# Kernel optimization log

Hardware: AMD Instinct MI355X
Metric: run time of the kernel (lower is better)

Reference implementation:

```python
import jax, jax.numpy as jnp
import numpy as np

# ---- configuration (matches init_kwargs) ----
B, C_IO, T = 2, 64, 4096
PATCH = 2
W0, W1 = 512, 1024           # widths
D_DN, D_MID = 2, 4           # depths per level
DH = 64                      # dim per head
WIN = 128                    # local attention window
MAP = 1024                   # mapping_dim
DFF_MAP = 1024               # mapping_d_ff
FF_MULT = 2                  # GEGLU ff_mult in local levels
H_DN = W0 // DH              # 8 heads
H_MID = W1 // DH             # 16 heads


def _n(key, shape, s=0.02):
    return jax.random.normal(key, shape, jnp.float32) * s


def setup_inputs() -> dict:
    key = jax.random.key(0)
    ks = iter(jax.random.split(key, 64))
    p = {}
    p['x'] = jax.random.normal(next(ks), (B, C_IO, T), jnp.float32)
    p['t'] = jax.random.uniform(next(ks), (B,), jnp.float32)
    p['time_w'] = jax.random.normal(next(ks), (MAP // 2, 1), jnp.float32)
    p['time_in_w'] = _n(next(ks), (MAP, MAP))
    p['map_in_s'] = jnp.ones((MAP,), jnp.float32)
    p['map_norm_s'] = jnp.ones((2, MAP), jnp.float32)
    p['map_up_w'] = _n(next(ks), (2, MAP, 2 * DFF_MAP))
    p['map_down_w'] = _n(next(ks), (2, DFF_MAP, MAP))
    p['map_out_s'] = jnp.ones((MAP,), jnp.float32)
    p['patch_in_w'] = _n(next(ks), (C_IO * PATCH, W0))
    p['dn_anorm_w'] = _n(next(ks), (D_DN, MAP, W0))
    p['dn_qkv_w'] = _n(next(ks), (D_DN, W0, 3 * W0))
    p['dn_o_w'] = _n(next(ks), (D_DN, W0, W0))
    p['dn_fnorm_w'] = _n(next(ks), (D_DN, MAP, W0))
    p['dn_ff1_w'] = _n(next(ks), (D_DN, W0, 2 * FF_MULT * W0))
    p['dn_ff2_w'] = _n(next(ks), (D_DN, FF_MULT * W0, W0))
    p['merge_w'] = _n(next(ks), (W0 * 2, W1))
    p['mid_map_w'] = _n(next(ks), (MAP, W1))
    p['mid_pin_w'] = _n(next(ks), (W1, W1))
    p['mid_pout_w'] = _n(next(ks), (W1, W1))
    p['mid_ln1_g'] = jnp.ones((D_MID, W1), jnp.float32)
    p['mid_ln1_b'] = jnp.zeros((D_MID, W1), jnp.float32)
    p['mid_qkv_w'] = _n(next(ks), (D_MID, W1, 3 * W1))
    p['mid_o_w'] = _n(next(ks), (D_MID, W1, W1))
    p['mid_ln2_g'] = jnp.ones((D_MID, W1), jnp.float32)
    p['mid_ln2_b'] = jnp.zeros((D_MID, W1), jnp.float32)
    p['mid_ff1_w'] = _n(next(ks), (D_MID, W1, 8 * W1))
    p['mid_ff2_w'] = _n(next(ks), (D_MID, 4 * W1, W1))
    p['mid_fn_g'] = jnp.ones((W1,), jnp.float32)
    p['mid_fn_b'] = jnp.zeros((W1,), jnp.float32)
    p['split_w'] = _n(next(ks), (W1, W0 * 2))
    p['split_fac'] = jnp.full((1,), 0.5, jnp.float32)
    p['up_anorm_w'] = _n(next(ks), (D_DN, MAP, W0))
    p['up_qkv_w'] = _n(next(ks), (D_DN, W0, 3 * W0))
    p['up_o_w'] = _n(next(ks), (D_DN, W0, W0))
    p['up_fnorm_w'] = _n(next(ks), (D_DN, MAP, W0))
    p['up_ff1_w'] = _n(next(ks), (D_DN, W0, 2 * FF_MULT * W0))
    p['up_ff2_w'] = _n(next(ks), (D_DN, FF_MULT * W0, W0))
    p['out_norm_s'] = jnp.ones((W0,), jnp.float32)
    p['patch_out_w'] = _n(next(ks), (W0, C_IO * PATCH))
    return p


def rmsnorm(x, scale, eps=1e-6):
    ms = jnp.mean(jnp.square(x), -1, keepdims=True)
    return x * (scale * jax.lax.rsqrt(ms + eps))


def layernorm(x, g, b, eps=1e-5):
    m = jnp.mean(x, -1, keepdims=True)
    v = jnp.mean(jnp.square(x - m), -1, keepdims=True)
    return (x - m) * jax.lax.rsqrt(v + eps) * g + b


def rope_tables(S, D):
    inv = 1.0 / (10000.0 ** (jnp.arange(0, D, 2, dtype=jnp.float32) / D))
    ang = jnp.arange(S, dtype=jnp.float32)[:, None] * inv  # [S, D/2]
    return jnp.cos(ang), jnp.sin(ang)


def apply_rope(x, cos, sin):
    # x: [B,H,S,D], contiguous-half rotation
    x1, x2 = jnp.split(x, 2, -1)
    return jnp.concatenate([x1 * cos - x2 * sin, x2 * cos + x1 * sin], -1)


def heads_split(x, h):
    Bx, S, C = x.shape
    return x.reshape(Bx, S, h, C // h).transpose(0, 2, 1, 3)


def heads_merge(x):
    Bx, h, S, D = x.shape
    return x.transpose(0, 2, 1, 3).reshape(Bx, S, h * D)


def local_attn(q, k, v, w):
    # non-causal sliding-window attention: each query window attends to
    # [prev, self, next] windows (look_backward=1, look_forward=1)
    Bx, H, S, D = q.shape
    nw = S // w
    qw = q.reshape(Bx, H, nw, w, D)
    def ctx(tn):
        tw = tn.reshape(Bx, H, nw, w, D)
        pad = jnp.pad(tw, ((0, 0), (0, 0), (1, 1), (0, 0), (0, 0)))
        return jnp.concatenate([pad[:, :, :-2], pad[:, :, 1:-1], pad[:, :, 2:]], 3)  # [B,H,nw,3w,D]
    kw, vw = ctx(k), ctx(v)
    s = jnp.einsum('bhnqd,bhnkd->bhnqk', qw * (D ** -0.5), kw)
    valid = jnp.ones((nw, 3 * w), bool).at[0, :w].set(False).at[-1, 2 * w:].set(False)
    s = jnp.where(valid[None, None, :, None, :], s, jnp.finfo(s.dtype).min)
    a = jax.nn.softmax(s, -1)
    return jnp.einsum('bhnqk,bhnkd->bhnqd', a, vw).reshape(Bx, H, S, D)


def token_merge(x, w, r=2):
    # 'b (n r) c -> b n (c r)' then linear
    Bx, S, C = x.shape
    x = x.reshape(Bx, S // r, r, C).transpose(0, 1, 3, 2).reshape(Bx, S // r, C * r)
    return x @ w


def token_split(x, w, r=2):
    # linear then 'b n (c r) -> b (n r) c'
    y = x @ w
    Bx, n, CR = y.shape
    C = CR // r
    return y.reshape(Bx, n, C, r).transpose(0, 1, 3, 2).reshape(Bx, n * r, C)


def mapping(e, in_s, norm_s, up_w, down_w, out_s):
    x = rmsnorm(e, in_s)
    for l in range(up_w.shape[0]):
        h = rmsnorm(x, norm_s[l])
        a, g = jnp.split(h @ up_w[l], 2, -1)
        x = x + (a * jax.nn.gelu(g)) @ down_w[l]
    return rmsnorm(x, out_s)


def local_level(x, cond, anorm, qkv_w, o_w, fnorm, ff1, ff2, heads, win):
    Bx, S, C = x.shape
    D = C // heads
    cos, sin = rope_tables(S, D)
    for l in range(qkv_w.shape[0]):
        h = rmsnorm(x, 1.0 + (cond @ anorm[l])[:, None, :])  # AdaRMSNorm
        q, k, v = jnp.split(h @ qkv_w[l], 3, -1)
        q, k, v = heads_split(q, heads), heads_split(k, heads), heads_split(v, heads)
        q, k = apply_rope(q, cos, sin), apply_rope(k, cos, sin)
        x = x + heads_merge(local_attn(q, k, v, win)) @ o_w[l]
        h = rmsnorm(x, 1.0 + (cond @ fnorm[l])[:, None, :])
        a, g = jnp.split(h @ ff1[l], 2, -1)
        x = x + (a * jax.nn.gelu(g)) @ ff2[l]  # GEGLU FF
    return x


def mid_level(x, ln1g, ln1b, qkv_w, o_w, ln2g, ln2b, ff1, ff2, fng, fnb, heads):
    Bx, S, C = x.shape
    D = C // heads
    cos, sin = rope_tables(S, D)
    for l in range(qkv_w.shape[0]):
        h = layernorm(x, ln1g[l], ln1b[l])
        q, k, v = jnp.split(h @ qkv_w[l], 3, -1)
        q, k, v = heads_split(q, heads), heads_split(k, heads), heads_split(v, heads)
        q, k = apply_rope(q, cos, sin), apply_rope(k, cos, sin)
        s = jnp.einsum('bhqd,bhkd->bhqk', q * (D ** -0.5), k)
        o = jnp.einsum('bhqk,bhkd->bhqd', jax.nn.softmax(s, -1), v)
        x = x + heads_merge(o) @ o_w[l]
        h = layernorm(x, ln2g[l], ln2b[l])
        a, g = jnp.split(h @ ff1[l], 2, -1)
        x = x + (a * jax.nn.silu(g)) @ ff2[l]  # SwiGLU FF
    return layernorm(x, fng, fnb)


def _forward(x, t, time_w, time_in_w, map_in_s, map_norm_s, map_up_w, map_down_w, map_out_s,
             patch_in_w, dn_anorm_w, dn_qkv_w, dn_o_w, dn_fnorm_w, dn_ff1_w, dn_ff2_w,
             merge_w, mid_map_w, mid_pin_w, mid_pout_w, mid_ln1_g, mid_ln1_b, mid_qkv_w,
             mid_o_w, mid_ln2_g, mid_ln2_b, mid_ff1_w, mid_ff2_w, mid_fn_g, mid_fn_b,
             split_w, split_fac, up_anorm_w, up_qkv_w, up_o_w, up_fnorm_w, up_ff1_w,
             up_ff2_w, out_norm_s, patch_out_w):
    h = jnp.swapaxes(x, 1, 2)                      # [B,T,C_io]
    h = token_merge(h, patch_in_w, PATCH)          # [B, T/2, W0]
    f = 2.0 * jnp.pi * (t[:, None] @ time_w.T)     # Fourier features
    temb = jnp.concatenate([jnp.cos(f), jnp.sin(f)], -1) @ time_in_w
    cond = mapping(temb, map_in_s, map_norm_s, map_up_w, map_down_w, map_out_s)  # [B,MAP]
    h = local_level(h, cond, dn_anorm_w, dn_qkv_w, dn_o_w, dn_fnorm_w, dn_ff1_w, dn_ff2_w, H_DN, WIN)
    skip = h
    h = token_merge(h, merge_w)                    # [B, T/4, W1]
    h = h @ mid_pin_w
    pre = (cond @ mid_map_w)[:, None, :]           # prepended mapping token
    h = jnp.concatenate([pre, h], 1)
    h = mid_level(h, mid_ln1_g, mid_ln1_b, mid_qkv_w, mid_o_w, mid_ln2_g, mid_ln2_b,
                  mid_ff1_w, mid_ff2_w, mid_fn_g, mid_fn_b, H_MID)
    h = (h @ mid_pout_w)[:, 1:, :]
    h = token_split(h, split_w)                    # back to [B, T/2, W0]
    h = skip + split_fac * (h - skip)              # lerp skip fusion
    h = local_level(h, cond, up_anorm_w, up_qkv_w, up_o_w, up_fnorm_w, up_ff1_w, up_ff2_w, H_DN, WIN)
    h = rmsnorm(h, out_norm_s)
    h = token_split(h, patch_out_w, PATCH)         # [B,T,C_io]
    return jnp.swapaxes(h, 1, 2)


def reference(x, t, time_w, time_in_w, map_in_s, map_norm_s, map_up_w, map_down_w, map_out_s,
              patch_in_w, dn_anorm_w, dn_qkv_w, dn_o_w, dn_fnorm_w, dn_ff1_w, dn_ff2_w,
              merge_w, mid_map_w, mid_pin_w, mid_pout_w, mid_ln1_g, mid_ln1_b, mid_qkv_w,
              mid_o_w, mid_ln2_g, mid_ln2_b, mid_ff1_w, mid_ff2_w, mid_fn_g, mid_fn_b,
              split_w, split_fac, up_anorm_w, up_qkv_w, up_o_w, up_fnorm_w, up_ff1_w,
              up_ff2_w, out_norm_s, patch_out_w):
    return _forward(x, t, time_w, time_in_w, map_in_s, map_norm_s, map_up_w, map_down_w, map_out_s,
                    patch_in_w, dn_anorm_w, dn_qkv_w, dn_o_w, dn_fnorm_w, dn_ff1_w, dn_ff2_w,
                    merge_w, mid_map_w, mid_pin_w, mid_pout_w, mid_ln1_g, mid_ln1_b, mid_qkv_w,
                    mid_o_w, mid_ln2_g, mid_ln2_b, mid_ff1_w, mid_ff2_w, mid_fn_g, mid_fn_b,
                    split_w, split_fac, up_anorm_w, up_qkv_w, up_o_w, up_fnorm_w, up_ff1_w,
                    up_ff2_w, out_norm_s, patch_out_w)
```

## Files before the change

kernel.cpp:

```cpp
#include <hip/hip_runtime.h>
#include <math.h>

#define BB   2
#define CIO  64
#define TT   4096
#define S0   2048
#define W0   512
#define HDN  8
#define SM   1025
#define SMP  1088
#define W1   1024
#define HMID 16
#define WIN  128
#define NW   16
#define MAPD 1024
#define KSPL 16
#define PKCAP 8396800L

typedef _Float16 f16;
typedef _Float16 half8 __attribute__((ext_vector_type(8)));
typedef _Float16 half4v __attribute__((ext_vector_type(4)));
typedef _Float16 half2v __attribute__((ext_vector_type(2)));
typedef float floatx4 __attribute__((ext_vector_type(4)));

__device__ __forceinline__ float gelu_tanh(float x) {
    float x3 = x * x * x;
    return 0.5f * x * (1.f + tanhf(0.7978845608028654f * (x + 0.044715f * x3)));
}

__global__ __launch_bounds__(256) void wcast(
    const float* __restrict__ W, f16* __restrict__ Wt, int K, int N) {
    __shared__ float T[64][65];
    const int n0 = blockIdx.x * 64, k0 = blockIdx.y * 64;
    const int tid = threadIdx.x;
    for (int e = tid; e < 4096; e += 256) {
        int r = e >> 6, c = e & 63;
        T[r][c] = W[(size_t)(k0 + r) * N + n0 + c];
    }
    __syncthreads();
    for (int e = tid; e < 2048; e += 256) {
        int r = e >> 5, c2 = (e & 31) * 2;
        half2v p;
        p[0] = (f16)T[c2][r];
        p[1] = (f16)T[c2 + 1][r];
        *(half2v*)(Wt + (size_t)(n0 + r) * K + k0 + c2) = p;
    }
}

template<int OUTM>
__global__ __launch_bounds__(256) void gemm_h(
    const f16* __restrict__ A, const f16* __restrict__ Bt,
    const float* __restrict__ res, void* __restrict__ Cv,
    int M, int N, int K) {
    __shared__ __align__(16) f16 As[3][4096];
    __shared__ __align__(16) f16 Bs[3][4096];
    const int tid = threadIdx.x;
    const int wv = tid >> 6, ln = tid & 63;
    int nwg = gridDim.x * gridDim.y;
    int orig = blockIdx.y * gridDim.x + blockIdx.x;
    int wg = orig;
    if (nwg >= 16) {
        int q = nwg >> 3, r = nwg & 7;
        int xcd = orig & 7, lot = orig >> 3;
        wg = (xcd < r ? xcd * (q + 1) : r * (q + 1) + (xcd - r) * q) + lot;
    }
    const int bm = (wg / gridDim.x) * 128, bn = (wg % gridDim.x) * 128;
    int Kc = K, kbase = 0;
    if (OUTM == 2) { Kc = K / gridDim.z; kbase = blockIdx.z * Kc; }
    const int nt = Kc >> 5;

    auto stage = [&](int buf, int kt) {
        int k0 = kbase + (kt << 5);
#pragma unroll
        for (int i = 0; i < 2; ++i) {
            int off = i * 4096 + wv * 1024 + ln * 16;
            int row = off >> 6, kb = (off & 63) >> 1;
            int gr = bm + row; gr = gr < M ? gr : M - 1;
            f16* gp = const_cast<f16*>(A) + (size_t)gr * K + k0 + kb;
            __builtin_amdgcn_global_load_lds(
                (__attribute__((address_space(1))) void*)gp,
                (__attribute__((address_space(3))) void*)(&As[buf][i * 2048 + wv * 512]),
                16, 0, 0);
            f16* gq = const_cast<f16*>(Bt) + (size_t)(bn + row) * K + k0 + kb;
            __builtin_amdgcn_global_load_lds(
                (__attribute__((address_space(1))) void*)gq,
                (__attribute__((address_space(3))) void*)(&Bs[buf][i * 2048 + wv * 512]),
                16, 0, 0);
        }
    };

    floatx4 acc[4][4];
#pragma unroll
    for (int m = 0; m < 4; ++m)
#pragma unroll
        for (int n = 0; n < 4; ++n) acc[m][n] = (floatx4)0.f;
    const int r = ln & 15, kc = (ln >> 4) * 8;
    const int wr = (wv >> 1) * 64, wc = (wv & 1) * 64;

    stage(0, 0);
    if (nt > 1) stage(1, 1);
    int buf = 0;
    for (int t = 0; t < nt; ++t) {
        if (t + 1 < nt) { asm volatile("s_waitcnt vmcnt(4)" ::: "memory"); }
        else            { asm volatile("s_waitcnt vmcnt(0)" ::: "memory"); }
        __builtin_amdgcn_s_barrier();
        if (t + 2 < nt) {
            int nb = buf + 2; if (nb >= 3) nb -= 3;
            stage(nb, t + 2);
        }
        half8 af[4], bf[4];
#pragma unroll
        for (int m = 0; m < 4; ++m)
            af[m] = *(const half8*)(&As[buf][(wr + m * 16 + r) * 32 + kc]);
#pragma unroll
        for (int n = 0; n < 4; ++n)
            bf[n] = *(const half8*)(&Bs[buf][(wc + n * 16 + r) * 32 + kc]);
#pragma unroll
        for (int m = 0; m < 4; ++m)
#pragma unroll
            for (int n = 0; n < 4; ++n)
                acc[m][n] = __builtin_amdgcn_mfma_f32_16x16x32_f16(af[m], bf[n], acc[m][n], 0, 0, 0);
        if (++buf >= 3) buf = 0;
    }

    float* Cf = (float*)Cv;
    f16*   Ch = (f16*)Cv;
    if (OUTM == 2) Cf += (size_t)blockIdx.z * M * N;
#pragma unroll
    for (int m = 0; m < 4; ++m) {
        int rbase = bm + wr + m * 16 + ((ln >> 4) << 2);
#pragma unroll
        for (int j = 0; j < 4; ++j) {
            int row = rbase + j;
            if (row < M) {
                size_t ro = (size_t)row * N;
#pragma unroll
                for (int n = 0; n < 4; ++n) {
                    int col = bn + wc + n * 16 + (ln & 15);
                    float v = acc[m][n][j];
                    if (OUTM == 1) Ch[ro + col] = (f16)v;
                    else if (OUTM == 0) Cf[ro + col] = v + (res ? res[ro + col] : 0.f);
                    else Cf[ro + col] = v;
                }
            }
        }
    }
}

__global__ __launch_bounds__(256) void gemm_qkv(
    const f16* __restrict__ A, const f16* __restrict__ Bt,
    const float* __restrict__ tab, f16* __restrict__ Fq,
    f16* __restrict__ Fk, f16* __restrict__ Fv,
    int M, int N, int K, int S, int H) {
    __shared__ __align__(16) f16 As[3][4096];
    __shared__ __align__(16) f16 Bs[3][4096];
    const int tid = threadIdx.x;
    const int wv = tid >> 6, ln = tid & 63;
    int nwg = gridDim.x * gridDim.y;
    int orig = blockIdx.y * gridDim.x + blockIdx.x;
    int wg = orig;
    if (nwg >= 16) {
        int q = nwg >> 3, r = nwg & 7;
        int xcd = orig & 7, lot = orig >> 3;
        wg = (xcd < r ? xcd * (q + 1) : r * (q + 1) + (xcd - r) * q) + lot;
    }
    const int bm = (wg / gridDim.x) * 128, bn = (wg % gridDim.x) * 128;
    const int nt = K >> 5;

    auto stage = [&](int buf, int kt) {
        int k0 = kt << 5;
#pragma unroll
        for (int i = 0; i < 2; ++i) {
            int off = i * 4096 + wv * 1024 + ln * 16;
            int row = off >> 6, kb = (off & 63) >> 1;
            int gr = bm + row; gr = gr < M ? gr : M - 1;
            f16* gp = const_cast<f16*>(A) + (size_t)gr * K + k0 + kb;
            __builtin_amdgcn_global_load_lds(
                (__attribute__((address_space(1))) void*)gp,
                (__attribute__((address_space(3))) void*)(&As[buf][i * 2048 + wv * 512]),
                16, 0, 0);
            f16* gq = const_cast<f16*>(Bt) + (size_t)(bn + row) * K + k0 + kb;
            __builtin_amdgcn_global_load_lds(
                (__attribute__((address_space(1))) void*)gq,
                (__attribute__((address_space(3))) void*)(&Bs[buf][i * 2048 + wv * 512]),
                16, 0, 0);
        }
    };

    floatx4 acc[4][4];
#pragma unroll
    for (int m = 0; m < 4; ++m)
#pragma unroll
        for (int n = 0; n < 4; ++n) acc[m][n] = (floatx4)0.f;
    const int r = ln & 15, kc = (ln >> 4) * 8;
    const int wr = (wv >> 1) * 64, wc = (wv & 1) * 64;

    stage(0, 0);
    if (nt > 1) stage(1, 1);
    int buf = 0;
    for (int t = 0; t < nt; ++t) {
        if (t + 1 < nt) { asm volatile("s_waitcnt vmcnt(4)" ::: "memory"); }
        else            { asm volatile("s_waitcnt vmcnt(0)" ::: "memory"); }
        __builtin_amdgcn_s_barrier();
        if (t + 2 < nt) {
            int nb = buf + 2; if (nb >= 3) nb -= 3;
            stage(nb, t + 2);
        }
        half8 af[4], bf[4];
#pragma unroll
        for (int m = 0; m < 4; ++m)
            af[m] = *(const half8*)(&As[buf][(wr + m * 16 + r) * 32 + kc]);
#pragma unroll
        for (int n = 0; n < 4; ++n)
            bf[n] = *(const half8*)(&Bs[buf][(wc + n * 16 + r) * 32 + kc]);
#pragma unroll
        for (int m = 0; m < 4; ++m)
#pragma unroll
            for (int n = 0; n < 4; ++n)
                acc[m][n] = __builtin_amdgcn_mfma_f32_16x16x32_f16(af[m], bf[n], acc[m][n], 0, 0, 0);
        if (++buf >= 3) buf = 0;
    }

    const int C = N / 3;
    const int colbase = bn + wc;
    const int reg = colbase / C;
// ... 120 lines not shown
    }
    P[((size_t)blockIdx.y * 2 + 0) * tot + c] = acc0;
    P[((size_t)blockIdx.y * 2 + 1) * tot + c] = acc1;
}

__global__ __launch_bounds__(256) void gemv2L_red(
    const float* __restrict__ P, float* __restrict__ C, int Nper, int L) {
    int tot = L * Nper;
    int g = blockIdx.x * 256 + threadIdx.x;
    if (g >= 2 * tot) return;
    int m = g / tot, cc = g - m * tot;
    float s = 0.f;
#pragma unroll
    for (int ky = 0; ky < KSPL; ++ky)
        s += P[((size_t)ky * 2 + m) * tot + cc];
    int l = cc / Nper, n = cc - l * Nper;
    C[((size_t)l * 2 + m) * Nper + n] = s;
}

__device__ __forceinline__ void stf(float* p, float v) { *p = v; }
__device__ __forceinline__ void stf(f16* p, float v)   { *p = (f16)v; }

template<typename TO>
__global__ __launch_bounds__(256) void rmsnorm_k(
    const float* __restrict__ X, const float* __restrict__ scale,
    TO* __restrict__ Y, int C, int rows_per_group, float sadd) {
    int row = blockIdx.x, tid = threadIdx.x;
    const float* x = X + (size_t)row * C;
    float v[8];
    int cnt = C >> 8;
    float ss = 0.f;
    for (int i = 0; i < cnt; ++i) { v[i] = x[tid + (i << 8)]; ss += v[i] * v[i]; }
    __shared__ float red[256];
    red[tid] = ss; __syncthreads();
    for (int s2 = 128; s2; s2 >>= 1) { if (tid < s2) red[tid] += red[tid + s2]; __syncthreads(); }
    float inv = rsqrtf(red[0] / (float)C + 1e-6f);
    const float* sc = scale + (size_t)(row / rows_per_group) * C;
    TO* y = Y + (size_t)row * C;
    for (int i = 0; i < cnt; ++i) {
        int c = tid + (i << 8);
        stf(&y[c], v[i] * (sadd + sc[c]) * inv);
    }
}

__global__ __launch_bounds__(256) void layernorm_k(
    const float* __restrict__ X, const float* __restrict__ g,
    const float* __restrict__ bta, f16* __restrict__ Y, int C) {
    int row = blockIdx.x, tid = threadIdx.x;
    const float* x = X + (size_t)row * C;
    float v[8];
    int cnt = C >> 8;
    float s = 0.f;
    for (int i = 0; i < cnt; ++i) { v[i] = x[tid + (i << 8)]; s += v[i]; }
    __shared__ float red[256];
    red[tid] = s; __syncthreads();
    for (int s2 = 128; s2; s2 >>= 1) { if (tid < s2) red[tid] += red[tid + s2]; __syncthreads(); }
    float m = red[0] / (float)C;
    __syncthreads();
    float s2s = 0.f;
    for (int i = 0; i < cnt; ++i) { float d = v[i] - m; s2s += d * d; }
    red[tid] = s2s; __syncthreads();
    for (int s2 = 128; s2; s2 >>= 1) { if (tid < s2) red[tid] += red[tid + s2]; __syncthreads(); }
    float inv = rsqrtf(red[0] / (float)C + 1e-5f);
    f16* y = Y + (size_t)row * C;
    for (int i = 0; i < cnt; ++i) {
        int c = tid + (i << 8);
        y[c] = (f16)((v[i] - m) * inv * g[c] + bta[c]);
    }
}

__global__ __launch_bounds__(256) void glu_k(
    const float* __restrict__ U, float* __restrict__ Yo,
    size_t total, int F, int mode) {
    size_t gidx = (size_t)blockIdx.x * 256 + threadIdx.x;
    if (gidx >= total) return;
    size_t r = gidx / (size_t)F;
    int c = (int)(gidx - r * F);
    const float* u = U + r * (size_t)(2 * F);
    float a = u[c], gg = u[F + c];
    float act = (mode == 0) ? gelu_tanh(gg) : gg / (1.f + expf(-gg));
    Yo[gidx] = a * act;
}

__global__ __launch_bounds__(256) void glu_h8(
    const f16* __restrict__ U, f16* __restrict__ Yo,
    size_t total8, int F8, int mode) {
    size_t gi = (size_t)blockIdx.x * 256 + threadIdx.x;
    if (gi >= total8) return;
    size_t r = gi / (size_t)F8;
    int c = (int)(gi - r * (size_t)F8);
    const f16* u = U + r * (size_t)F8 * 16;
    half8 av = *(const half8*)(u + c * 8);
    half8 gv = *(const half8*)(u + F8 * 8 + c * 8);
    half8 y;
#pragma unroll
    for (int j = 0; j < 8; ++j) {
        float a = (float)av[j], gg = (float)gv[j];
        float act = (mode == 0) ? gelu_tanh(gg) : gg / (1.f + __expf(-gg));
        y[j] = (f16)(a * act);
    }
    *(half8*)(Yo + gi * 8) = y;
}

__global__ __launch_bounds__(256) void vtrans(
    const f16* __restrict__ V, f16* __restrict__ Vt, int S, int Spad) {
    __shared__ f16 T[64][72];
    const int tid = threadIdx.x;
    const int k0 = blockIdx.x * 64;
    const f16* Vb = V + (size_t)blockIdx.y * S * 64;
    f16* Vtb = Vt + (size_t)blockIdx.y * 64 * Spad;
    for (int c = tid; c < 512; c += 256) {
        int kk = c >> 3, d8 = (c & 7) * 8;
        int kg = k0 + kk; kg = kg < S ? kg : S - 1;
        half8 v = *(const half8*)(Vb + (size_t)kg * 64 + d8);
        if (k0 + kk >= S) {
#pragma unroll
            for (int j = 0; j < 8; ++j) v[j] = (f16)0.f;
        }
        *(half8*)(&T[kk][d8]) = v;
    }
    __syncthreads();
    for (int c = tid; c < 512; c += 256) {
        int d = c >> 3, k8 = (c & 7) * 8;
        half8 o;
#pragma unroll
        for (int j = 0; j < 8; ++j) o[j] = T[k8 + j][d];
        *(half8*)(Vtb + (size_t)d * Spad + k0 + k8) = o;
    }
}

__global__ __launch_bounds__(256) void fattn(
    const f16* __restrict__ Q, const f16* __restrict__ K,
    const f16* __restrict__ Vt, float* __restrict__ Op,
    float* __restrict__ Mst, float* __restrict__ Lst,
    int S, int Spad, int H, int win, int QR) {
    __shared__ __align__(16) f16 Ks[64][72];
    __shared__ __align__(16) f16 Vs[64][72];
    __shared__ __align__(16) f16 Ps[4][32][72];
    const int tid = threadIdx.x;
    const int wv = tid >> 6, ln = tid & 63;
    const int r15 = ln & 15, g = ln >> 4;
    const int bh = blockIdx.y;
    const int NBH = gridDim.y;
    const int z = blockIdx.z, nz = gridDim.z;
    const int q0 = (int)blockIdx.x * 128;
    const f16* Qb = Q + (size_t)bh * S * 64;
    const f16* Kb = K + (size_t)bh * S * 64;
    const f16* Vtb = Vt + (size_t)bh * 64 * Spad;

    half8 aq[2][2];
#pragma unroll
    for (int m = 0; m < 2; ++m) {
        int q = q0 + wv * 32 + m * 16 + r15;
        q = q < S ? q : S - 1;
#pragma unroll
        for (int ks = 0; ks < 2; ++ks)
            aq[m][ks] = *(const half8*)(Qb + (size_t)q * 64 + ks * 32 + g * 8);
    }
    floatx4 o[2][4];
#pragma unroll
    for (int m = 0; m < 2; ++m)
#pragma unroll
        for (int n = 0; n < 4; ++n) o[m][n] = (floatx4)0.f;
    float mst[2][4], lst[2][4];
#pragma unroll
    for (int m = 0; m < 2; ++m)
#pragma unroll
        for (int j = 0; j < 4; ++j) { mst[m][j] = -3.0e38f; lst[m][j] = 0.f; }

    int klo = 0, khi = S;
    if (win) {
        int n = (int)blockIdx.x;
        klo = (n - 1) * win; if (klo < 0) klo = 0;
        khi = (n + 2) * win; if (khi > S) khi = S;
    }
    int ntile = (khi - klo + 63) >> 6;
    int chunk = (ntile + nz - 1) / nz;
    int myLo = klo + z * chunk * 64;
    int myHi = klo + (z + 1) * chunk * 64; if (myHi > khi) myHi = khi;

    for (int kb = myLo; kb < myHi; kb += 64) {
        __syncthreads();
#pragma unroll
        for (int i = 0; i < 2; ++i) {
            int c = tid + i * 256;
            int rr = c >> 3, c8 = (c & 7) * 8;
            int kg = kb + rr; kg = kg < S ? kg : S - 1;
            *(half8*)(&Ks[rr][c8]) = *(const half8*)(Kb + (size_t)kg * 64 + c8);
            *(half8*)(&Vs[rr][c8]) = *(const half8*)(Vtb + (size_t)rr * Spad + kb + c8);
        }
        __syncthreads();
        floatx4 s[2][4];
#pragma unroll
        for (int m = 0; m < 2; ++m)
#pragma unroll
            for (int n = 0; n < 4; ++n) s[m][n] = (floatx4)0.f;
#pragma unroll
        for (int ks = 0; ks < 2; ++ks) {
            half8 bk[4];
#pragma unroll
            for (int n = 0; n < 4; ++n)
                bk[n] = *(const half8*)(&Ks[n * 16 + r15][ks * 32 + g * 8]);
#pragma unroll
            for (int m = 0; m < 2; ++m)
#pragma unroll
                for (int n = 0; n < 4; ++n)
                    s[m][n] = __builtin_amdgcn_mfma_f32_16x16x32_f16(aq[m][ks], bk[n], s[m][n], 0, 0, 0);
        }
        if (kb + 64 > S) {
#pragma unroll
            for (int n = 0; n < 4; ++n)
                if (kb + n * 16 + r15 >= S) {
#pragma unroll
                    for (int m = 0; m < 2; ++m) s[m][n] = (floatx4)(-3.0e38f);
                }
        }
#pragma unroll
        for (int m = 0; m < 2; ++m) {
#pragma unroll
            for (int j = 0; j < 4; ++j) {
                float tm = fmaxf(fmaxf(s[m][0][j], s[m][1][j]), fmaxf(s[m][2][j], s[m][3][j]));
                tm = fmaxf(tm, __shfl_xor(tm, 1));
                tm = fmaxf(tm, __shfl_xor(tm, 2));
                tm = fmaxf(tm, __shfl_xor(tm, 4));
                tm = fmaxf(tm, __shfl_xor(tm, 8));
                float mn = fmaxf(mst[m][j], tm);
                float sc = __expf(mst[m][j] - mn);
                mst[m][j] = mn;
                float ts = 0.f;
#pragma unroll
                for (int n = 0; n < 4; ++n) {
                    float p = __expf(s[m][n][j] - mn);
                    s[m][n][j] = p;
                    ts += p;
                }
                ts += __shfl_xor(ts, 1);
                ts += __shfl_xor(ts, 2);
                ts += __shfl_xor(ts, 4);
                ts += __shfl_xor(ts, 8);
                lst[m][j] = lst[m][j] * sc + ts;
#pragma unroll
                for (int n = 0; n < 4; ++n) o[m][n][j] *= sc;
            }
        }
#pragma unroll
        for (int m = 0; m < 2; ++m)
#pragma unroll
            for (int n = 0; n < 4; ++n)
#pragma unroll
                for (int j = 0; j < 4; ++j)
                    Ps[wv][m * 16 + g * 4 + j][n * 16 + r15] = (f16)s[m][n][j];
#pragma unroll
        for (int ks = 0; ks < 2; ++ks) {
            half8 pa[2], bv[4];
#pragma unroll
            for (int m = 0; m < 2; ++m)
                pa[m] = *(const half8*)(&Ps[wv][m * 16 + r15][ks * 32 + g * 8]);
#pragma unroll
            for (int n = 0; n < 4; ++n)
                bv[n] = *(const half8*)(&Vs[n * 16 + r15][ks * 32 + g * 8]);
#pragma unroll
            for (int m = 0; m < 2; ++m)
#pragma unroll
                for (int n = 0; n < 4; ++n)
                    o[m][n] = __builtin_amdgcn_mfma_f32_16x16x32_f16(pa[m], bv[n], o[m][n], 0, 0, 0);
        }
    }
    size_t zb = ((size_t)z * NBH + bh) * QR;
#pragma unroll
    for (int m = 0; m < 2; ++m)
#pragma unroll
        for (int j = 0; j < 4; ++j) {
            int qr = q0 + wv * 32 + m * 16 + g * 4 + j;
            size_t ro = (zb + qr) * 64;
#pragma unroll
            for (int n = 0; n < 4; ++n)
                Op[ro + n * 16 + r15] = o[m][n][j];
            if (r15 == 0) {
                Mst[zb + qr] = mst[m][j];
                Lst[zb + qr] = lst[m][j];
            }
        }
}

__global__ __launch_bounds__(256) void fcomb(
    const float* __restrict__ Op, const float* __restrict__ Mst,
    const float* __restrict__ Lst, f16* __restrict__ O,
    int S, int H, int QR, int nz, int rows) {
    int g = blockIdx.x * 256 + threadIdx.x;
    int idx = g >> 4;
    int d4 = (g & 15) * 4;
    if (idx >= rows) return;
    int bh = idx / QR, q = idx - bh * QR;
    if (q >= S) return;
    float mstar = -3.0e38f;
    for (int z = 0; z < nz; ++z)
        mstar = fmaxf(mstar, Mst[(size_t)z * rows + idx]);
    float den = 0.f;
    floatx4 num = (floatx4)0.f;
    for (int z = 0; z < nz; ++z) {
        float w = __expf(Mst[(size_t)z * rows + idx] - mstar);
        den += w * Lst[(size_t)z * rows + idx];
        floatx4 ov = *(const floatx4*)(Op + ((size_t)z * rows + idx) * 64 + d4);
        num += w * ov;
    }
    float inv = 1.f / den;
    int b = bh / H, h = bh % H;
    f16* op = O + ((size_t)b * S + q) * (H * 64) + h * 64 + d4;
    half4v hv;
#pragma unroll
    for (int j = 0; j < 4; ++j) hv[j] = (f16)(num[j] * inv);
    *(half4v*)op = hv;
}

__global__ __launch_bounds__(256) void patch_in_gather(
    const float* __restrict__ x, f16* __restrict__ out) {
    int g = blockIdx.x * 256 + threadIdx.x;
    if (g >= BB * S0 * 128) return;
    int k = g & 127;
    int n = (g >> 7) & (S0 - 1);
    int b = g >> 18;
    out[g] = (f16)x[(size_t)b * CIO * TT + (size_t)(k >> 1) * TT + 2 * n + (k & 1)];
}

__global__ __launch_bounds__(256) void time_embed(
    const float* __restrict__ t, const float* __restrict__ tw,
    float* __restrict__ te) {
    int g = blockIdx.x * 256 + threadIdx.x;
    if (g >= BB * MAPD) return;
    int b = g / MAPD, j = g % MAPD;
    float w = tw[(j < 512) ? j : j - 512];
    float ang = 6.283185307179586f * t[b] * w;
    te[g] = (j < 512) ? cosf(ang) : sinf(ang);
}

__global__ __launch_bounds__(256) void token_merge_gather(
    const float* __restrict__ A, f16* __restrict__ out) {
    int g = blockIdx.x * 256 + threadIdx.x;
    if (g >= BB * 1024 * 1024) return;
    int k = g & 1023;
    int n = (g >> 10) & 1023;
    int b = g >> 20;
    out[g] = (f16)A[((size_t)b * S0 + 2 * n + (k & 1)) * W0 + (k >> 1)];
}

__global__ __launch_bounds__(256) void concat_mid(
    const float* __restrict__ pre, const float* __restrict__ Dsrc,
    float* __restrict__ Cm) {
    int g = blockIdx.x * 256 + threadIdx.x;
    if (g >= BB * SM * W1) return;
    int c = g & 1023;
    int row = g >> 10;
    int b = row / SM, r = row % SM;
    Cm[g] = (r == 0) ? pre[b * W1 + c]
                     : Dsrc[((size_t)b * 1024 + r - 1) * W1 + c];
}

__global__ __launch_bounds__(256) void gather_drop(
    const f16* __restrict__ Dsrc, f16* __restrict__ out) {
    int g = blockIdx.x * 256 + threadIdx.x;
    if (g >= BB * 1024 * W1) return;
    int c = g & 1023;
    int n = (g >> 10) & 1023;
    int b = g >> 20;
    out[g] = Dsrc[((size_t)b * SM + 1 + n) * W1 + c];
// ... 24 lines not shown

extern "C" void kernel_launch(void* const* d_in, const int* in_sizes, int n_in,
                              void* d_out, int out_size, void* d_ws, size_t ws_size,
                              hipStream_t stream) {
    const float* x          = (const float*)d_in[0];
    const float* t          = (const float*)d_in[1];
    const float* time_w     = (const float*)d_in[2];
    const float* time_in_w  = (const float*)d_in[3];
    const float* map_in_s   = (const float*)d_in[4];
    const float* map_norm_s = (const float*)d_in[5];
    const float* map_up_w   = (const float*)d_in[6];
    const float* map_down_w = (const float*)d_in[7];
    const float* map_out_s  = (const float*)d_in[8];
    const float* patch_in_w = (const float*)d_in[9];
    const float* dn_anorm_w = (const float*)d_in[10];
    const float* dn_qkv_w   = (const float*)d_in[11];
    const float* dn_o_w     = (const float*)d_in[12];
    const float* dn_fnorm_w = (const float*)d_in[13];
    const float* dn_ff1_w   = (const float*)d_in[14];
    const float* dn_ff2_w   = (const float*)d_in[15];
    const float* merge_w    = (const float*)d_in[16];
    const float* mid_map_w  = (const float*)d_in[17];
    const float* mid_pin_w  = (const float*)d_in[18];
    const float* mid_pout_w = (const float*)d_in[19];
    const float* mid_ln1_g  = (const float*)d_in[20];
    const float* mid_ln1_b  = (const float*)d_in[21];
    const float* mid_qkv_w  = (const float*)d_in[22];
    const float* mid_o_w    = (const float*)d_in[23];
    const float* mid_ln2_g  = (const float*)d_in[24];
    const float* mid_ln2_b  = (const float*)d_in[25];
    const float* mid_ff1_w  = (const float*)d_in[26];
    const float* mid_ff2_w  = (const float*)d_in[27];
    const float* mid_fn_g   = (const float*)d_in[28];
    const float* mid_fn_b   = (const float*)d_in[29];
    const float* split_w    = (const float*)d_in[30];
    const float* split_fac  = (const float*)d_in[31];
    const float* up_anorm_w = (const float*)d_in[32];
    const float* up_qkv_w   = (const float*)d_in[33];
    const float* up_o_w     = (const float*)d_in[34];
    const float* up_fnorm_w = (const float*)d_in[35];
    const float* up_ff1_w   = (const float*)d_in[36];
    const float* up_ff2_w   = (const float*)d_in[37];
    const float* out_norm_s = (const float*)d_in[38];
    const float* patch_out_w= (const float*)d_in[39];

    float* Wp = (float*)d_ws;
    size_t off = 0;
    auto alloc = [&](size_t n) { float* p = Wp + off; off += n; return p; };
    float* A    = alloc((size_t)4096 * 512);
    float* Bsk  = alloc((size_t)4096 * 512);
    float* Cm   = alloc((size_t)2050 * 1024);
    float* Df   = alloc((size_t)2050 * 1024);
    f16*  Fq    = (f16*)alloc((size_t)1049600);
    f16*  Fk    = (f16*)alloc((size_t)1049600);
    f16*  Fv    = (f16*)alloc((size_t)1049600);
    f16*  Fvt   = (f16*)alloc((size_t)1114112);
    f16*  H1    = (f16*)alloc((size_t)8396800);
    f16*  H2    = (f16*)alloc((size_t)4198400);
    f16*  Wh    = (f16*)alloc((size_t)4194304);
    float* Pk   = alloc((size_t)PKCAP);
    float* ML   = alloc((size_t)262144);
    float* Pb   = alloc((size_t)KSPL * 2 * 2048);
    float* tabL = alloc((size_t)S0 * 64);
    float* tabM = alloc((size_t)SM * 64);
    float* Sma  = alloc((size_t)32768);
    (void)ws_size; (void)in_sizes; (void)n_in; (void)out_size;

    float* te   = Sma;
    float* temb = Sma + 2048;
    float* mapx = Sma + 4096;
    float* maph = Sma + 6144;
    float* mapu = Sma + 8192;
    float* mapg = Sma + 12288;
    float* cond = Sma + 14336;
    float* pre  = Sma + 18432;
    float* sAdn = Sma + 20480;
    float* sFdn = Sma + 22528;
    float* sAup = Sma + 24576;
    float* sFup = Sma + 26624;

    auto WC = [&](const float* W, int K, int N) {
        wcast<<<dim3(N / 64, K / 64), 256, 0, stream>>>(W, Wh, K, N);
    };
    auto pick_ks = [](int M, int N, int K) {
        long gx = N / 128, gy = (M + 127) / 128;
        int ks = 1;
        while (gx * gy * ks < 512 && ks < 8) {
            int nk = ks * 2;
            if ((K / nk) % 32 != 0 || (long)M * N * nk > PKCAP) break;
            ks = nk;
        }
        return ks;
    };
    auto GF = [&](const f16* Aa, const float* res, float* C, int M, int N, int K) {
        int ks = pick_ks(M, N, K);
        dim3 g(N / 128, (M + 127) / 128, ks);
        if (ks == 1) {
            gemm_h<0><<<g, 256, 0, stream>>>(Aa, Wh, res, C, M, N, K);
        } else {
            gemm_h<2><<<g, 256, 0, stream>>>(Aa, Wh, nullptr, Pk, M, N, K);
            size_t mn = (size_t)M * N;
            kred<false><<<(int)((mn / 4 + 255) / 256), 256, 0, stream>>>(Pk, res, C, mn, ks);
        }
    };
    auto GH = [&](const f16* Aa, f16* C, int M, int N, int K) {
        int ks = pick_ks(M, N, K);
        dim3 g(N / 128, (M + 127) / 128, ks);
        if (ks == 1) {
            gemm_h<1><<<g, 256, 0, stream>>>(Aa, Wh, nullptr, C, M, N, K);
        } else {
            gemm_h<2><<<g, 256, 0, stream>>>(Aa, Wh, nullptr, Pk, M, N, K);
            size_t mn = (size_t)M * N;
            kred<true><<<(int)((mn / 4 + 255) / 256), 256, 0, stream>>>(Pk, nullptr, C, mn, ks);
        }
    };
    auto GQKV = [&](const f16* Aa, const float* tab, int M, int N, int K, int S, int H) {
        dim3 g(N / 128, (M + 127) / 128);
        gemm_qkv<<<g, 256, 0, stream>>>(Aa, Wh, tab, Fq, Fk, Fv, M, N, K, S, H);
    };
    auto gemv2 = [&](const float* Aa, const float* W, const float* res,
                     float* C, int N, int K) {
        gemv2_part<<<dim3((N + 255) / 256, KSPL), 256, 0, stream>>>(Aa, W, Pb, N, K);
        gemv2_red<<<(2 * N + 255) / 256, 256, 0, stream>>>(Pb, res, C, N);
    };
    auto gemv2L = [&](const float* Aa, const float* W, float* C, int Nper, int L, int K) {
        int tot = L * Nper;
        gemv2L_part<<<dim3((tot + 255) / 256, KSPL), 256, 0, stream>>>(Aa, W, Pb, Nper, L, K);
        gemv2L_red<<<(2 * tot + 255) / 256, 256, 0, stream>>>(Pb, C, Nper, L);
    };
    auto FATT = [&](const f16* Qp, const f16* Kp, const f16* Vtp, f16* Out,
                    int S, int Spad, int H, int win, int nq, int nbh, int nz) {
        int QR = nq * 128;
        int rows = nbh * QR;
        fattn<<<dim3(nq, nbh, nz), 256, 0, stream>>>(
            Qp, Kp, Vtp, Pk, ML, ML + (size_t)nz * rows, S, Spad, H, win, QR);
        fcomb<<<(rows * 16 + 255) / 256, 256, 0, stream>>>(
            Pk, ML, ML + (size_t)nz * rows, Out, S, H, QR, nz, rows);
    };

    rope_tab<<<(S0 * 32 + 255) / 256, 256, 0, stream>>>(tabL, S0);
    rope_tab<<<(SM * 32 + 255) / 256, 256, 0, stream>>>(tabM, SM);

    patch_in_gather<<<(BB * S0 * 128 + 255) / 256, 256, 0, stream>>>(x, H2);
    WC(patch_in_w, 128, 512);
    GF(H2, nullptr, A, 4096, 512, 128);

    time_embed<<<(BB * MAPD + 255) / 256, 256, 0, stream>>>(t, time_w, te);
    gemv2(te, time_in_w, nullptr, temb, 1024, 1024);
    rmsnorm_k<float><<<2, 256, 0, stream>>>(temb, map_in_s, mapx, 1024, 2, 0.f);
    for (int l = 0; l < 2; ++l) {
        rmsnorm_k<float><<<2, 256, 0, stream>>>(mapx, map_norm_s + (size_t)l * 1024, maph, 1024, 2, 0.f);
        gemv2(maph, map_up_w + (size_t)l * 1024 * 2048, nullptr, mapu, 2048, 1024);
        glu_k<<<(2 * 1024 + 255) / 256, 256, 0, stream>>>(mapu, mapg, 2 * 1024, 1024, 0);
        gemv2(mapg, map_down_w + (size_t)l * 1024 * 1024, mapx, mapx, 1024, 1024);
    }
    rmsnorm_k<float><<<2, 256, 0, stream>>>(mapx, map_out_s, cond, 1024, 2, 0.f);

    gemv2L(cond, dn_anorm_w, sAdn, 512, 2, 1024);
    gemv2L(cond, dn_fnorm_w, sFdn, 512, 2, 1024);
    gemv2L(cond, up_anorm_w, sAup, 512, 2, 1024);
    gemv2L(cond, up_fnorm_w, sFup, 512, 2, 1024);
    gemv2L(cond, mid_map_w,  pre, 1024, 1, 1024);

    auto run_local = [&](const float* qkvw, const float* ow,
                         const float* ff1, const float* ff2,
                         const float* sAall, const float* sFall) {
        for (int l = 0; l < 2; ++l) {
            rmsnorm_k<f16><<<4096, 256, 0, stream>>>(A, sAall + (size_t)l * 1024, H2, 512, 2048, 1.f);
            WC(qkvw + (size_t)l * 512 * 1536, 512, 1536);
            GQKV(H2, tabL, 4096, 1536, 512, S0, HDN);
            vtrans<<<dim3(S0 / 64, BB * HDN), 256, 0, stream>>>(Fv, Fvt, S0, S0);
            FATT(Fq, Fk, Fvt, H2, S0, S0, HDN, WIN, S0 / 128, BB * HDN, 2);
            WC(ow + (size_t)l * 512 * 512, 512, 512);
            GF(H2, A, A, 4096, 512, 512);
            rmsnorm_k<f16><<<4096, 256, 0, stream>>>(A, sFall + (size_t)l * 1024, H2, 512, 2048, 1.f);
            WC(ff1 + (size_t)l * 512 * 2048, 512, 2048);
            GH(H2, H1, 4096, 2048, 512);
            glu_h8<<<(4096 * 128 + 255) / 256, 256, 0, stream>>>(H1, H2, (size_t)4096 * 128, 128, 0);
            WC(ff2 + (size_t)l * 1024 * 512, 1024, 512);
            GF(H2, A, A, 4096, 512, 1024);
        }
    };
    run_local(dn_qkv_w, dn_o_w, dn_ff1_w, dn_ff2_w, sAdn, sFdn);

    hipMemcpyAsync(Bsk, A, (size_t)4096 * 512 * 4, hipMemcpyDeviceToDevice, stream);
    token_merge_gather<<<(BB * 1024 * 1024 + 255) / 256, 256, 0, stream>>>(A, H2);
    WC(merge_w, 1024, 1024);
    GH(H2, H1, 2048, 1024, 1024);
    WC(mid_pin_w, 1024, 1024);
    GF(H1, nullptr, Df, 2048, 1024, 1024);
    concat_mid<<<(BB * SM * W1 + 255) / 256, 256, 0, stream>>>(pre, Df, Cm);

    for (int l = 0; l < 4; ++l) {
        layernorm_k<<<2050, 256, 0, stream>>>(Cm, mid_ln1_g + (size_t)l * 1024,
                                              mid_ln1_b + (size_t)l * 1024, H2, 1024);
        WC(mid_qkv_w + (size_t)l * 1024 * 3072, 1024, 3072);
        GQKV(H2, tabM, 2050, 3072, 1024, SM, HMID);
        vtrans<<<dim3(SMP / 64, BB * HMID), 256, 0, stream>>>(Fv, Fvt, SM, SMP);
        FATT(Fq, Fk, Fvt, H2, SM, SMP, HMID, 0, 9, BB * HMID, 3);
        WC(mid_o_w + (size_t)l * 1024 * 1024, 1024, 1024);
        GF(H2, Cm, Cm, 2050, 1024, 1024);
        layernorm_k<<<2050, 256, 0, stream>>>(Cm, mid_ln2_g + (size_t)l * 1024,
                                              mid_ln2_b + (size_t)l * 1024, H2, 1024);
        WC(mid_ff1_w + (size_t)l * 1024 * 8192, 1024, 8192);
        GH(H2, H1, 2050, 8192, 1024);
        glu_h8<<<(int)(((size_t)2050 * 512 + 255) / 256), 256, 0, stream>>>(H1, H2, (size_t)2050 * 512, 512, 1);
        WC(mid_ff2_w + (size_t)l * 4096 * 1024, 4096, 1024);
        GF(H2, Cm, Cm, 2050, 1024, 4096);
    }
    layernorm_k<<<2050, 256, 0, stream>>>(Cm, mid_fn_g, mid_fn_b, H2, 1024);

    WC(mid_pout_w, 1024, 1024);
    GH(H2, H1, 2050, 1024, 1024);
    gather_drop<<<(BB * 1024 * W1 + 255) / 256, 256, 0, stream>>>(H1, H2);
    WC(split_w, 1024, 1024);
    GF(H2, nullptr, Df, 2048, 1024, 1024);
    split_scatter_lerp<<<(BB * S0 * W0 + 255) / 256, 256, 0, stream>>>(Df, Bsk, split_fac, A);

    run_local(up_qkv_w, up_o_w, up_ff1_w, up_ff2_w, sAup, sFup);

    rmsnorm_k<f16><<<4096, 256, 0, stream>>>(A, out_norm_s, H2, 512, 4096, 0.f);
    WC(patch_out_w, 512, 128);
    GF(H2, nullptr, Df, 4096, 128, 512);
    patch_out_scatter<<<(BB * CIO * TT + 255) / 256, 256, 0, stream>>>(Df, (float*)d_out);
}
```

Baseline: 2.101 ms.

## Fuse GLU into FF1 GEMM epilogue and write local attention output directly

Adds a weight-cast kernel that interleaves value and gate columns so each 128-wide GEMM tile holds matching value/gate pairs. The GEMM epilogue then applies GELU/SiLU and writes the half-width fp16 output, which removes the separate GLU kernel and the full-width intermediate write and read. Local windowed attention now runs without a K-split, using 64-row query blocks and normalising in the epilogue, so the fcomb pass and the fp32 partial buffers are skipped. The mid attention is templated with scheduling-priority hints around the MFMA loops. The risk is a lower occupancy or a layout mismatch in the interleaved weights.

```diff
diff --git a/kernel.cpp b/kernel.cpp
--- a/kernel.cpp
+++ b/kernel.cpp
@@ -47,11 +47,34 @@
     }
 }
 
+__global__ __launch_bounds__(256) void wcast_glu(
+    const float* __restrict__ W, f16* __restrict__ Wt, int K, int F2) {
+    __shared__ float T[64][65];
+    const int F = F2 >> 1;
+    const int n0 = blockIdx.x * 64, k0 = blockIdx.y * 64;
+    const int tid = threadIdx.x;
+    for (int e = tid; e < 4096; e += 256) {
+        int r = e >> 6, c = e & 63;
+        int oc = (c < 32) ? (n0 / 2 + c) : (F + n0 / 2 + (c - 32));
+        T[r][c] = W[(size_t)(k0 + r) * F2 + oc];
+    }
+    __syncthreads();
+    for (int e = tid; e < 2048; e += 256) {
+        int rr = e >> 5, c2 = (e & 31) * 2;
+        int pl = rr >> 5, i = rr & 31;
+        int tc = (i < 16) ? (pl * 16 + i) : (32 + pl * 16 + (i - 16));
+        half2v p;
+        p[0] = (f16)T[c2][tc];
+        p[1] = (f16)T[c2 + 1][tc];
+        *(half2v*)(Wt + (size_t)(n0 + rr) * K + k0 + c2) = p;
+    }
+}
+
 template<int OUTM>
 __global__ __launch_bounds__(256) void gemm_h(
     const f16* __restrict__ A, const f16* __restrict__ Bt,
     const float* __restrict__ res, void* __restrict__ Cv,
-    int M, int N, int K) {
+    int M, int N, int K, int glumode) {
     __shared__ __align__(16) f16 As[3][4096];
     __shared__ __align__(16) f16 Bs[3][4096];
     const int tid = threadIdx.x;
@@ -126,6 +149,7 @@
     float* Cf = (float*)Cv;
     f16*   Ch = (f16*)Cv;
     if (OUTM == 2) Cf += (size_t)blockIdx.z * M * N;
+    const int base2 = (bn + wc) >> 1;
 #pragma unroll
     for (int m = 0; m < 4; ++m) {
         int rbase = bm + wr + m * 16 + ((ln >> 4) << 2);
@@ -133,14 +157,25 @@
         for (int j = 0; j < 4; ++j) {
             int row = rbase + j;
             if (row < M) {
-                size_t ro = (size_t)row * N;
-#pragma unroll
-                for (int n = 0; n < 4; ++n) {
-                    int col = bn + wc + n * 16 + (ln & 15);
-                    float v = acc[m][n][j];
-                    if (OUTM == 1) Ch[ro + col] = (f16)v;
-                    else if (OUTM == 0) Cf[ro + col] = v + (res ? res[ro + col] : 0.f);
-                    else Cf[ro + col] = v;
+                if (OUTM == 3) {
+                    size_t ro = (size_t)row * (N >> 1);
+#pragma unroll
+                    for (int k = 0; k < 2; ++k) {
+                        float a = acc[m][2 * k][j], gg = acc[m][2 * k + 1][j];
+                        float act = (glumode == 0) ? gelu_tanh(gg)
+                                                   : gg / (1.f + __expf(-gg));
+                        Ch[ro + base2 + k * 16 + (ln & 15)] = (f16)(a * act);
+                    }
+                } else {
+                    size_t ro = (size_t)row * N;
+#pragma unroll
+                    for (int n = 0; n < 4; ++n) {
+                        int col = bn + wc + n * 16 + (ln & 15);
+                        float v = acc[m][n][j];
+                        if (OUTM == 1) Ch[ro + col] = (f16)v;
+                        else if (OUTM == 0) Cf[ro + col] = v + (res ? res[ro + col] : 0.f);
+                        else Cf[ro + col] = v;
+                    }
                 }
             }
         }
@@ -427,26 +462,6 @@
     Yo[gidx] = a * act;
 }
 
-__global__ __launch_bounds__(256) void glu_h8(
-    const f16* __restrict__ U, f16* __restrict__ Yo,
-    size_t total8, int F8, int mode) {
-    size_t gi = (size_t)blockIdx.x * 256 + threadIdx.x;
-    if (gi >= total8) return;
-    size_t r = gi / (size_t)F8;
-    int c = (int)(gi - r * (size_t)F8);
-    const f16* u = U + r * (size_t)F8 * 16;
-    half8 av = *(const half8*)(u + c * 8);
-    half8 gv = *(const half8*)(u + F8 * 8 + c * 8);
-    half8 y;
-#pragma unroll
-    for (int j = 0; j < 8; ++j) {
-        float a = (float)av[j], gg = (float)gv[j];
-        float act = (mode == 0) ? gelu_tanh(gg) : gg / (1.f + __expf(-gg));
-        y[j] = (f16)(a * act);
-    }
-    *(half8*)(Yo + gi * 8) = y;
-}
-
 __global__ __launch_bounds__(256) void vtrans(
     const f16* __restrict__ V, f16* __restrict__ Vt, int S, int Spad) {
     __shared__ f16 T[64][72];
@@ -474,10 +489,11 @@
     }
 }
 
+template<int MF, bool DIRECT>
 __global__ __launch_bounds__(256) void fattn(
     const f16* __restrict__ Q, const f16* __restrict__ K,
     const f16* __restrict__ Vt, float* __restrict__ Op,
-    float* __restrict__ Mst, float* __restrict__ Lst,
+    float* __restrict__ Mst, float* __restrict__ Lst, f16* __restrict__ O,
     int S, int Spad, int H, int win, int QR) {
     __shared__ __align__(16) f16 Ks[64][72];
     __shared__ __align__(16) f16 Vs[64][72];
@@ -488,36 +504,36 @@
     const int bh = blockIdx.y;
     const int NBH = gridDim.y;
     const int z = blockIdx.z, nz = gridDim.z;
-    const int q0 = (int)blockIdx.x * 128;
+    const int q0 = (int)blockIdx.x * (MF * 64);
     const f16* Qb = Q + (size_t)bh * S * 64;
     const f16* Kb = K + (size_t)bh * S * 64;
     const f16* Vtb = Vt + (size_t)bh * 64 * Spad;
 
-    half8 aq[2][2];
-#pragma unroll
-    for (int m = 0; m < 2; ++m) {
-        int q = q0 + wv * 32 + m * 16 + r15;
+    half8 aq[MF][2];
+#pragma unroll
+    for (int m = 0; m < MF; ++m) {
+        int q = q0 + wv * (MF * 16) + m * 16 + r15;
         q = q < S ? q : S - 1;
 #pragma unroll
         for (int ks = 0; ks < 2; ++ks)
             aq[m][ks] = *(const half8*)(Qb + (size_t)q * 64 + ks * 32 + g * 8);
     }
-    floatx4 o[2][4];
-#pragma unroll
-    for (int m = 0; m < 2; ++m)
+    floatx4 o[MF][4];
+#pragma unroll
+    for (int m = 0; m < MF; ++m)
 #pragma unroll
         for (int n = 0; n < 4; ++n) o[m][n] = (floatx4)0.f;
-    float mst[2][4], lst[2][4];
-#pragma unroll
-    for (int m = 0; m < 2; ++m)
+    float mst[MF][4], lst[MF][4];
+#pragma unroll
+    for (int m = 0; m < MF; ++m)
 #pragma unroll
         for (int j = 0; j < 4; ++j) { mst[m][j] = -3.0e38f; lst[m][j] = 0.f; }
 
     int klo = 0, khi = S;
     if (win) {
-        int n = (int)blockIdx.x;
-        klo = (n - 1) * win; if (klo < 0) klo = 0;
-        khi = (n + 2) * win; if (khi > S) khi = S;
+        int wb = q0 >> 7;
+        klo = (wb - 1) * win; if (klo < 0) klo = 0;
+        khi = (wb + 2) * win; if (khi > S) khi = S;
     }
     int ntile = (khi - klo + 63) >> 6;
     int chunk = (ntile + nz - 1) / nz;
@@ -535,11 +551,12 @@
             *(half8*)(&Vs[rr][c8]) = *(const half8*)(Vtb + (size_t)rr * Spad + kb + c8);
         }
         __syncthreads();
-        floatx4 s[2][4];
-#pragma unroll
-        for (int m = 0; m < 2; ++m)
+        floatx4 s[MF][4];
+#pragma unroll
+        for (int m = 0; m < MF; ++m)
 #pragma unroll
             for (int n = 0; n < 4; ++n) s[m][n] = (floatx4)0.f;
+        __builtin_amdgcn_s_setprio(1);
 #pragma unroll
         for (int ks = 0; ks < 2; ++ks) {
             half8 bk[4];
@@ -547,21 +564,22 @@
             for (int n = 0; n < 4; ++n)
                 bk[n] = *(const half8*)(&Ks[n * 16 + r15][ks * 32 + g * 8]);
 #pragma unroll
-            for (int m = 0; m < 2; ++m)
+            for (int m = 0; m < MF; ++m)
 #pragma unroll
                 for (int n = 0; n < 4; ++n)
                     s[m][n] = __builtin_amdgcn_mfma_f32_16x16x32_f16(aq[m][ks], bk[n], s[m][n], 0, 0, 0);
         }
+        __builtin_amdgcn_s_setprio(0);
         if (kb + 64 > S) {
 #pragma unroll
             for (int n = 0; n < 4; ++n)
                 if (kb + n * 16 + r15 >= S) {
 #pragma unroll
-                    for (int m = 0; m < 2; ++m) s[m][n] = (floatx4)(-3.0e38f);
+                    for (int m = 0; m < MF; ++m) s[m][n] = (floatx4)(-3.0e38f);
                 }
         }
 #pragma unroll
-        for (int m = 0; m < 2; ++m) {
+        for (int m = 0; m < MF; ++m) {
 #pragma unroll
             for (int j = 0; j < 4; ++j) {
                 float tm = fmaxf(fmaxf(s[m][0][j], s[m][1][j]), fmaxf(s[m][2][j], s[m][3][j]));
@@ -589,43 +607,63 @@
             }
         }
 #pragma unroll
-        for (int m = 0; m < 2; ++m)
+        for (int m = 0; m < MF; ++m)
 #pragma unroll
             for (int n = 0; n < 4; ++n)
 #pragma unroll
                 for (int j = 0; j < 4; ++j)
                     Ps[wv][m * 16 + g * 4 + j][n * 16 + r15] = (f16)s[m][n][j];
+        __builtin_amdgcn_s_setprio(1);
 #pragma unroll
         for (int ks = 0; ks < 2; ++ks) {
-            half8 pa[2], bv[4];
-#pragma unroll
-            for (int m = 0; m < 2; ++m)
+            half8 pa[MF], bv[4];
+#pragma unroll
+            for (int m = 0; m < MF; ++m)
                 pa[m] = *(const half8*)(&Ps[wv][m * 16 + r15][ks * 32 + g * 8]);
 #pragma unroll
             for (int n = 0; n < 4; ++n)
                 bv[n] = *(const half8*)(&Vs[n * 16 + r15][ks * 32 + g * 8]);
 #pragma unroll
-            for (int m = 0; m < 2; ++m)
+            for (int m = 0; m < MF; ++m)
 #pragma unroll
                 for (int n = 0; n < 4; ++n)
                     o[m][n] = __builtin_amdgcn_mfma_f32_16x16x32_f16(pa[m], bv[n], o[m][n], 0, 0, 0);
         }
-    }
-    size_t zb = ((size_t)z * NBH + bh) * QR;
-#pragma unroll
-    for (int m = 0; m < 2; ++m)
-#pragma unroll
-        for (int j = 0; j < 4; ++j) {
-            int qr = q0 + wv * 32 + m * 16 + g * 4 + j;
-            size_t ro = (zb + qr) * 64;
-#pragma unroll
-            for (int n = 0; n < 4; ++n)
-                Op[ro + n * 16 + r15] = o[m][n][j];
-            if (r15 == 0) {
-                Mst[zb + qr] = mst[m][j];
-                Lst[zb + qr] = lst[m][j];
+        __builtin_amdgcn_s_setprio(0);
+    }
+    if (DIRECT) {
+        const int HC = H * 64;
+        const int b = bh / H, h = bh % H;
+#pragma unroll
+        for (int m = 0; m < MF; ++m)
+#pragma unroll
+            for (int j = 0; j < 4; ++j) {
+                int q = q0 + wv * (MF * 16) + m * 16 + g * 4 + j;
+                if (q < S) {
+                    float inv = 1.f / lst[m][j];
+                    size_t ro = ((size_t)b * S + q) * HC + h * 64;
+#pragma unroll
+                    for (int n = 0; n < 4; ++n)
+                        O[ro + n * 16 + r15] = (f16)(o[m][n][j] * inv);
+                }
             }
-        }
+    } else {
+        size_t zb = ((size_t)z * NBH + bh) * QR;
+#pragma unroll
+        for (int m = 0; m < MF; ++m)
+#pragma unroll
+            for (int j = 0; j < 4; ++j) {
+                int qr = q0 + wv * (MF * 16) + m * 16 + g * 4 + j;
+                size_t ro = (zb + qr) * 64;
+#pragma unroll
+                for (int n = 0; n < 4; ++n)
+                    Op[ro + n * 16 + r15] = o[m][n][j];
+                if (r15 == 0) {
+                    Mst[zb + qr] = mst[m][j];
+                    Lst[zb + qr] = lst[m][j];
+                }
+            }
+    }
 }
 
 __global__ __launch_bounds__(256) void fcomb(
@@ -816,6 +854,9 @@
     auto WC = [&](const float* W, int K, int N) {
         wcast<<<dim3(N / 64, K / 64), 256, 0, stream>>>(W, Wh, K, N);
     };
+    auto WCG = [&](const float* W, int K, int N2) {
+        wcast_glu<<<dim3(N2 / 64, K / 64), 256, 0, stream>>>(W, Wh, K, N2);
+    };
     auto pick_ks = [](int M, int N, int K) {
         long gx = N / 128, gy = (M + 127) / 128;
         int ks = 1;
@@ -830,9 +871,9 @@
         int ks = pick_ks(M, N, K);
         dim3 g(N / 128, (M + 127) / 128, ks);
         if (ks == 1) {
-            gemm_h<0><<<g, 256, 0, stream>>>(Aa, Wh, res, C, M, N, K);
+            gemm_h<0><<<g, 256, 0, stream>>>(Aa, Wh, res, C, M, N, K, 0);
         } else {
-            gemm_h<2><<<g, 256, 0, stream>>>(Aa, Wh, nullptr, Pk, M, N, K);
+            gemm_h<2><<<g, 256, 0, stream>>>(Aa, Wh, nullptr, Pk, M, N, K, 0);
             size_t mn = (size_t)M * N;
             kred<false><<<(int)((mn / 4 + 255) / 256), 256, 0, stream>>>(Pk, res, C, mn, ks);
         }
@@ -841,12 +882,16 @@
         int ks = pick_ks(M, N, K);
         dim3 g(N / 128, (M + 127) / 128, ks);
         if (ks == 1) {
-            gemm_h<1><<<g, 256, 0, stream>>>(Aa, Wh, nullptr, C, M, N, K);
+            gemm_h<1><<<g, 256, 0, stream>>>(Aa, Wh, nullptr, C, M, N, K, 0);
         } else {
-            gemm_h<2><<<g, 256, 0, stream>>>(Aa, Wh, nullptr, Pk, M, N, K);
+            gemm_h<2><<<g, 256, 0, stream>>>(Aa, Wh, nullptr, Pk, M, N, K, 0);
             size_t mn = (size_t)M * N;
             kred<true><<<(int)((mn / 4 + 255) / 256), 256, 0, stream>>>(Pk, nullptr, C, mn, ks);
         }
+    };
+    auto GGLU = [&](const f16* Aa, f16* C, int M, int N2, int K, int mode) {
+        dim3 g(N2 / 128, (M + 127) / 128);
+        gemm_h<3><<<g, 256, 0, stream>>>(Aa, Wh, nullptr, C, M, N2, K, mode);
     };
     auto GQKV = [&](const f16* Aa, const float* tab, int M, int N, int K, int S, int H) {
         dim3 g(N / 128, (M + 127) / 128);
@@ -861,15 +906,6 @@
         int tot = L * Nper;
         gemv2L_part<<<dim3((tot + 255) / 256, KSPL), 256, 0, stream>>>(Aa, W, Pb, Nper, L, K);
         gemv2L_red<<<(2 * tot + 255) / 256, 256, 0, stream>>>(Pb, C, Nper, L);
-    };
-    auto FATT = [&](const f16* Qp, const f16* Kp, const f16* Vtp, f16* Out,
-                    int S, int Spad, int H, int win, int nq, int nbh, int nz) {
-        int QR = nq * 128;
-        int rows = nbh * QR;
-        fattn<<<dim3(nq, nbh, nz), 256, 0, stream>>>(
-            Qp, Kp, Vtp, Pk, ML, ML + (size_t)nz * rows, S, Spad, H, win, QR);
-        fcomb<<<(rows * 16 + 255) / 256, 256, 0, stream>>>(
-            Pk, ML, ML + (size_t)nz * rows, Out, S, H, QR, nz, rows);
     };
 
     rope_tab<<<(S0 * 32 + 255) / 256, 256, 0, stream>>>(tabL, S0);
@@ -904,15 +940,15 @@
             WC(qkvw + (size_t)l * 512 * 1536, 512, 1536);
             GQKV(H2, tabL, 4096, 1536, 512, S0, HDN);
             vtrans<<<dim3(S0 / 64, BB * HDN), 256, 0, stream>>>(Fv, Fvt, S0, S0);
-            FATT(Fq, Fk, Fvt, H2, S0, S0, HDN, WIN, S0 / 128, BB * HDN, 2);
+            fattn<1, true><<<dim3(S0 / 64, BB * HDN, 1), 256, 0, stream>>>(
+                Fq, Fk, Fvt, nullptr, nullptr, nullptr, H2, S0, S0, HDN, WIN, 0);
             WC(ow + (size_t)l * 512 * 512, 512, 512);
             GF(H2, A, A, 4096, 512, 512);
             rmsnorm_k<f16><<<4096, 256, 0, stream>>>(A, sFall + (size_t)l * 1024, H2, 512, 2048, 1.f);
-            WC(ff1 + (size_t)l * 512 * 2048, 512, 2048);
-            GH(H2, H1, 4096, 2048, 512);
-            glu_h8<<<(4096 * 128 + 255) / 256, 256, 0, stream>>>(H1, H2, (size_t)4096 * 128, 128, 0);
+            WCG(ff1 + (size_t)l * 512 * 2048, 512, 2048);
+            GGLU(H2, H1, 4096, 2048, 512, 0);
             WC(ff2 + (size_t)l * 1024 * 512, 1024, 512);
-            GF(H2, A, A, 4096, 512, 1024);
+            GF(H1, A, A, 4096, 512, 1024);
         }
     };
     run_local(dn_qkv_w, dn_o_w, dn_ff1_w, dn_ff2_w, sAdn, sFdn);
@@ -931,16 +967,21 @@
         WC(mid_qkv_w + (size_t)l * 1024 * 3072, 1024, 3072);
         GQKV(H2, tabM, 2050, 3072, 1024, SM, HMID);
         vtrans<<<dim3(SMP / 64, BB * HMID), 256, 0, stream>>>(Fv, Fvt, SM, SMP);
-        FATT(Fq, Fk, Fvt, H2, SM, SMP, HMID, 0, 9, BB * HMID, 3);
+        {
+            int QR = 9 * 128, rows = BB * HMID * QR, nz = 3;
+            fattn<2, false><<<dim3(9, BB * HMID, nz), 256, 0, stream>>>(
+                Fq, Fk, Fvt, Pk, ML, ML + (size_t)nz * rows, nullptr, SM, SMP, HMID, 0, QR);
+            fcomb<<<(rows * 16 + 255) / 256, 256, 0, stream>>>(
+                Pk, ML, ML + (size_t)nz * rows, H2, SM, HMID, QR, nz, rows);
+        }
         WC(mid_o_w + (size_t)l * 1024 * 1024, 1024, 1024);
         GF(H2, Cm, Cm, 2050, 1024, 1024);
         layernorm_k<<<2050, 256, 0, stream>>>(Cm, mid_ln2_g + (size_t)l * 1024,
                                               mid_ln2_b + (size_t)l * 1024, H2, 1024);
-        WC(mid_ff1_w + (size_t)l * 1024 * 8192, 1024, 8192);
-        GH(H2, H1, 2050, 8192, 1024);
-        glu_h8<<<(int)(((size_t)2050 * 512 + 255) / 256), 256, 0, stream>>>(H1, H2, (size_t)2050 * 512, 512, 1);
+        WCG(mid_ff1_w + (size_t)l * 1024 * 8192, 1024, 8192);
+        GGLU(H2, H1, 2050, 8192, 1024, 1);
         WC(mid_ff2_w + (size_t)l * 4096 * 1024, 4096, 1024);
-        GF(H2, Cm, Cm, 2050, 1024, 4096);
+        GF(H1, Cm, Cm, 2050, 1024, 4096);
     }
     layernorm_k<<<2050, 256, 0, stream>>>(Cm, mid_fn_g, mid_fn_b, H2, 1024);
 
```

Measured after the change: 1.985 ms. 5.5% less time.
